# Kernel tuning notes

Measured on AMD Instinct MI355X. Metric: run time of the kernel, lower is better.

Reference implementation:

```python
import jax, jax.numpy as jnp
import numpy as np

LN2 = float(np.log(2.0))

def shifted_softplus(x):
    return jax.nn.softplus(x) - LN2

def setup_inputs() -> dict:
    key = jax.random.key(0)
    ks = jax.random.split(key, 6)
    B, N, K, G, F = 32, 256, 64, 64, 128
    features = jax.random.normal(ks[0], (B, N, F), dtype=jnp.float32)
    rbf_expansion = jax.random.uniform(ks[1], (B, N, K, G), dtype=jnp.float32)
    neighbor_list = jax.random.randint(ks[2], (B, N, K), 0, N).astype(jnp.int64)
    neighbor_mask = jnp.ones((B, N, K), dtype=jnp.float32)
    W1 = jax.random.normal(ks[3], (G, F), dtype=jnp.float32) * (1.0 / np.sqrt(G))
    b1 = jnp.zeros((F,), dtype=jnp.float32)
    W2 = jax.random.normal(ks[4], (F, F), dtype=jnp.float32) * (1.0 / np.sqrt(F))
    b2 = jnp.zeros((F,), dtype=jnp.float32)
    return {"features": features, "rbf_expansion": rbf_expansion,
            "neighbor_list": neighbor_list, "neighbor_mask": neighbor_mask,
            "W1": W1, "b1": b1, "W2": W2, "b2": b2}

def reference(features, rbf_expansion, neighbor_list, neighbor_mask, W1, b1, W2, b2):
    B, N, K = neighbor_list.shape
    F = features.shape[2]
    # filter-generating MLP: linear + shifted softplus, then linear (no activation)
    h = shifted_softplus(jnp.einsum('bnkg,gf->bnkf', rbf_expansion, W1) + b1)
    conv_filter = jnp.einsum('bnkf,fh->bnkh', h, W2) + b2  # [B,N,K,F]
    # gather neighbor features along bead axis
    idx = neighbor_list.reshape(B, N * K)[..., None]  # [B, N*K, 1]
    neighbor_features = jnp.take_along_axis(features, idx, axis=1).reshape(B, N, K, F)
    conv_features = neighbor_features * conv_filter * neighbor_mask[:, :, :, None]
    aggregated_features = jnp.sum(conv_features, axis=2)  # [B, N, F]
    return aggregated_features
```

## Files before the change

### kernel.cpp

```cpp
#include <hip/hip_runtime.h>

#define LN2f 0.69314718055994530942f

typedef short s16x8 __attribute__((ext_vector_type(8)));
typedef float f32x4 __attribute__((ext_vector_type(4)));

constexpr int Bdim = 32, Ndim = 256, Kn = 64, Gdim = 64, Fdim = 128;
constexpr int TPB = 8;
constexpr int LDH = Fdim + 8;

__device__ __forceinline__ short f2bf(float x) {
    unsigned u = __float_as_uint(x);
    u = (u + 0x7FFFu + ((u >> 16) & 1u)) >> 16;
    return (short)u;
}
__device__ __forceinline__ s16x8 cvt8(float4 u, float4 v) {
    s16x8 a;
    a[0]=f2bf(u.x); a[1]=f2bf(u.y); a[2]=f2bf(u.z); a[3]=f2bf(u.w);
    a[4]=f2bf(v.x); a[5]=f2bf(v.y); a[6]=f2bf(v.z); a[7]=f2bf(v.w);
    return a;
}

__global__ __launch_bounds__(256, 2)
void cfconv_kernel(const float* __restrict__ features,
                   const float* __restrict__ rbf,
                   const int*   __restrict__ nbr,
                   const float* __restrict__ mask,
                   const float* __restrict__ W1,
                   const float* __restrict__ b1,
                   const float* __restrict__ W2,
                   const float* __restrict__ b2,
                   float* __restrict__ out)
{
    __shared__ short h_lds[Kn][LDH];
    __shared__ int   nbr_lds[2][Kn];
    __shared__ float mask_lds[2][Kn];

    const int tid  = threadIdx.x;
    const int lane = tid & 63;
    const int w    = tid >> 6;
    const int l16  = lane & 15;
    const int grp  = lane >> 4;

    s16x8 w1f[2][2];
    #pragma unroll
    for (int ks = 0; ks < 2; ++ks)
      #pragma unroll
      for (int nf = 0; nf < 2; ++nf) {
        int g0 = ks*32 + grp*8;
        int f  = w*32 + nf*16 + l16;
        #pragma unroll
        for (int j = 0; j < 8; ++j)
          w1f[ks][nf][j] = f2bf(W1[(g0+j)*Fdim + f]);
      }
    s16x8 w2f[4][2];
    #pragma unroll
    for (int ks = 0; ks < 4; ++ks)
      #pragma unroll
      for (int nf = 0; nf < 2; ++nf) {
        int g0 = ks*32 + grp*8;
        int f  = w*32 + nf*16 + l16;
        #pragma unroll
        for (int j = 0; j < 8; ++j)
          w2f[ks][nf][j] = f2bf(W2[(g0+j)*Fdim + f]);
      }
    float b1v[2], b2v[2];
    #pragma unroll
    for (int nf = 0; nf < 2; ++nf) {
      int f = w*32 + nf*16 + l16;
      b1v[nf] = b1[f];
      b2v[nf] = b2[f];
    }

    const int bn0 = blockIdx.x * TPB;

    float4 st[8][2];
    {
        const float* rb = rbf + (size_t)bn0 * (Kn * Gdim) + l16 * Gdim + grp * 8;
        #pragma unroll
        for (int i = 0; i < 8; ++i) {
            const float* p = rb + (i >> 1) * 16 * Gdim + (i & 1) * 32;
            st[i][0] = *(const float4*)p;
            st[i][1] = *(const float4*)(p + 4);
        }
    }

    for (int t = 0; t < TPB; ++t) {
        const int bn = bn0 + t;
        const int b  = bn >> 8;

        if (tid < Kn) {
            nbr_lds[t & 1][tid]  = nbr[bn*Kn + tid];
            mask_lds[t & 1][tid] = mask[bn*Kn + tid];
        }

        s16x8 af[4][2];
        #pragma unroll
        for (int m = 0; m < 4; ++m) {
            af[m][0] = cvt8(st[m*2][0],   st[m*2][1]);
            af[m][1] = cvt8(st[m*2+1][0], st[m*2+1][1]);
        }
        if (t + 1 < TPB) {
            const float* rbn = rbf + (size_t)(bn + 1) * (Kn * Gdim) + l16 * Gdim + grp * 8;
            #pragma unroll
            for (int i = 0; i < 8; ++i) {
                const float* p = rbn + (i >> 1) * 16 * Gdim + (i & 1) * 32;
                st[i][0] = *(const float4*)p;
                st[i][1] = *(const float4*)(p + 4);
            }
        }

        f32x4 acc[4][2];
        #pragma unroll
        for (int m = 0; m < 4; ++m)
          #pragma unroll
          for (int nf = 0; nf < 2; ++nf)
            acc[m][nf] = (f32x4){0.f, 0.f, 0.f, 0.f};
        #pragma unroll
        for (int m = 0; m < 4; ++m)
          #pragma unroll
          for (int ks = 0; ks < 2; ++ks)
            #pragma unroll
            for (int nf = 0; nf < 2; ++nf)
              acc[m][nf] = __builtin_amdgcn_mfma_f32_16x16x32_bf16(
                               af[m][ks], w1f[ks][nf], acc[m][nf], 0, 0, 0);

        #pragma unroll
        for (int m = 0; m < 4; ++m)
          #pragma unroll
          for (int nf = 0; nf < 2; ++nf)
            #pragma unroll
            for (int r = 0; r < 4; ++r) {
              float x  = acc[m][nf][r] + b1v[nf];
              float sp = fmaxf(x, 0.f) + __logf(1.f + __expf(-fabsf(x))) - LN2f;
              int row = m*16 + grp*4 + r;
              int col = w*32 + nf*16 + l16;
              h_lds[row][col] = f2bf(sp);
            }
        __syncthreads();

        #pragma unroll
        for (int m = 0; m < 4; ++m)
          #pragma unroll
          for (int nf = 0; nf < 2; ++nf)
            acc[m][nf] = (f32x4){0.f, 0.f, 0.f, 0.f};
        #pragma unroll
        for (int m = 0; m < 4; ++m) {
          #pragma unroll
          for (int ks = 0; ks < 4; ++ks) {
            s16x8 a = *(const s16x8*)&h_lds[m*16 + l16][ks*32 + grp*8];
            #pragma unroll
            for (int nf = 0; nf < 2; ++nf)
              acc[m][nf] = __builtin_amdgcn_mfma_f32_16x16x32_bf16(
                               a, w2f[ks][nf], acc[m][nf], 0, 0, 0);
          }
        }
        __syncthreads();

        const float* fb = features + (size_t)b * (Ndim * Fdim);
        float o0 = 0.f, o1 = 0.f;
        #pragma unroll
        for (int m = 0; m < 4; ++m)
          #pragma unroll
          for (int r = 0; r < 4; ++r) {
            int   kn  = m*16 + grp*4 + r;
            int   idx = nbr_lds[t & 1][kn];
            float mk  = mask_lds[t & 1][kn];
            const float* fr = fb + idx * Fdim;
            int f0 = w*32 + l16;
            float flt0 = (acc[m][0][r] + b2v[0]) * mk;
            float flt1 = (acc[m][1][r] + b2v[1]) * mk;
            o0 += fr[f0]      * flt0;
            o1 += fr[f0 + 16] * flt1;
          }
        o0 += __shfl_xor(o0, 16); o0 += __shfl_xor(o0, 32);
        o1 += __shfl_xor(o1, 16); o1 += __shfl_xor(o1, 32);
        float ov = (grp == 0) ? o0 : o1;
        if (grp < 2)
            out[(size_t)bn * Fdim + w*32 + grp*16 + l16] = ov;
    }
}

extern "C" void kernel_launch(void* const* d_in, const int* in_sizes, int n_in,
                              void* d_out, int out_size, void* d_ws, size_t ws_size,
                              hipStream_t stream) {
    const float* features = (const float*)d_in[0];
    const float* rbf      = (const float*)d_in[1];
    const int*   nbr      = (const int*)  d_in[2];
    const float* mask     = (const float*)d_in[3];
    const float* W1       = (const float*)d_in[4];
    const float* b1       = (const float*)d_in[5];
    const float* W2       = (const float*)d_in[6];
    const float* b2       = (const float*)d_in[7];
    float* out = (float*)d_out;

    dim3 grid(Bdim * Ndim / TPB), block(256);
    hipLaunchKernelGGL(cfconv_kernel, grid, block, 0, stream,
                       features, rbf, nbr, mask, W1, b1, W2, b2, out);
}
```

Before: 269.2 us.

## Use packed bf16 convert and overlap neighbor gathers with second GEMM halves

Replaces the software float-to-bf16 rounding with the hardware v_cvt_pk_bf16_f32 instruction, packing two values per conversion. The second GEMM is split into two halves of rows, and the neighbor feature gathers for each half are issued before its MFMAs so global load latency hides behind matrix work. Accumulation uses split partial sums, and the trailing barrier moves to the end of the iteration. This adds register pressure for the prefetched gather values, which could affect occupancy under the launch bound of 2.

```diff
diff --git a/kernel.cpp b/kernel.cpp
--- a/kernel.cpp
+++ b/kernel.cpp
@@ -4,21 +4,21 @@
 
 typedef short s16x8 __attribute__((ext_vector_type(8)));
 typedef float f32x4 __attribute__((ext_vector_type(4)));
+typedef unsigned int u32;
+typedef unsigned int u32x4 __attribute__((ext_vector_type(4)));
 
 constexpr int Bdim = 32, Ndim = 256, Kn = 64, Gdim = 64, Fdim = 128;
 constexpr int TPB = 8;
 constexpr int LDH = Fdim + 8;
 
-__device__ __forceinline__ short f2bf(float x) {
-    unsigned u = __float_as_uint(x);
-    u = (u + 0x7FFFu + ((u >> 16) & 1u)) >> 16;
-    return (short)u;
+__device__ __forceinline__ u32 cvtpk(float lo, float hi) {
+    u32 r;
+    asm("v_cvt_pk_bf16_f32 %0, %1, %2" : "=v"(r) : "v"(lo), "v"(hi));
+    return r;
 }
 __device__ __forceinline__ s16x8 cvt8(float4 u, float4 v) {
-    s16x8 a;
-    a[0]=f2bf(u.x); a[1]=f2bf(u.y); a[2]=f2bf(u.z); a[3]=f2bf(u.w);
-    a[4]=f2bf(v.x); a[5]=f2bf(v.y); a[6]=f2bf(v.z); a[7]=f2bf(v.w);
-    return a;
+    u32x4 q = { cvtpk(u.x, u.y), cvtpk(u.z, u.w), cvtpk(v.x, v.y), cvtpk(v.z, v.w) };
+    return __builtin_bit_cast(s16x8, q);
 }
 
 __global__ __launch_bounds__(256, 2)
@@ -41,6 +41,7 @@
     const int w    = tid >> 6;
     const int l16  = lane & 15;
     const int grp  = lane >> 4;
+    const int f0   = w * 32 + l16;
 
     s16x8 w1f[2][2];
     #pragma unroll
@@ -49,9 +50,11 @@
       for (int nf = 0; nf < 2; ++nf) {
         int g0 = ks*32 + grp*8;
         int f  = w*32 + nf*16 + l16;
-        #pragma unroll
-        for (int j = 0; j < 8; ++j)
-          w1f[ks][nf][j] = f2bf(W1[(g0+j)*Fdim + f]);
+        u32x4 q;
+        #pragma unroll
+        for (int j2 = 0; j2 < 4; ++j2)
+          q[j2] = cvtpk(W1[(g0 + 2*j2)*Fdim + f], W1[(g0 + 2*j2 + 1)*Fdim + f]);
+        w1f[ks][nf] = __builtin_bit_cast(s16x8, q);
       }
     s16x8 w2f[4][2];
     #pragma unroll
@@ -60,9 +63,11 @@
       for (int nf = 0; nf < 2; ++nf) {
         int g0 = ks*32 + grp*8;
         int f  = w*32 + nf*16 + l16;
-        #pragma unroll
-        for (int j = 0; j < 8; ++j)
-          w2f[ks][nf][j] = f2bf(W2[(g0+j)*Fdim + f]);
+        u32x4 q;
+        #pragma unroll
+        for (int j2 = 0; j2 < 4; ++j2)
+          q[j2] = cvtpk(W2[(g0 + 2*j2)*Fdim + f], W2[(g0 + 2*j2 + 1)*Fdim + f]);
+        w2f[ks][nf] = __builtin_bit_cast(s16x8, q);
       }
     float b1v[2], b2v[2];
     #pragma unroll
@@ -88,10 +93,11 @@
     for (int t = 0; t < TPB; ++t) {
         const int bn = bn0 + t;
         const int b  = bn >> 8;
+        const int cb = t & 1;
 
         if (tid < Kn) {
-            nbr_lds[t & 1][tid]  = nbr[bn*Kn + tid];
-            mask_lds[t & 1][tid] = mask[bn*Kn + tid];
+            nbr_lds[cb][tid]  = nbr[bn*Kn + tid];
+            mask_lds[cb][tid] = mask[bn*Kn + tid];
         }
 
         s16x8 af[4][2];
@@ -128,56 +134,94 @@
         #pragma unroll
         for (int m = 0; m < 4; ++m)
           #pragma unroll
-          for (int nf = 0; nf < 2; ++nf)
-            #pragma unroll
-            for (int r = 0; r < 4; ++r) {
-              float x  = acc[m][nf][r] + b1v[nf];
-              float sp = fmaxf(x, 0.f) + __logf(1.f + __expf(-fabsf(x))) - LN2f;
-              int row = m*16 + grp*4 + r;
-              int col = w*32 + nf*16 + l16;
-              h_lds[row][col] = f2bf(sp);
-            }
+          for (int r = 0; r < 4; ++r) {
+            float x0 = acc[m][0][r] + b1v[0];
+            float x1 = acc[m][1][r] + b1v[1];
+            float s0 = fmaxf(x0, 0.f) + __logf(1.f + __expf(-fabsf(x0))) - LN2f;
+            float s1 = fmaxf(x1, 0.f) + __logf(1.f + __expf(-fabsf(x1))) - LN2f;
+            u32 p = cvtpk(s0, s1);
+            int row = m*16 + grp*4 + r;
+            h_lds[row][f0]      = (short)(p & 0xffffu);
+            h_lds[row][f0 + 16] = (short)(p >> 16);
+          }
         __syncthreads();
 
-        #pragma unroll
-        for (int m = 0; m < 4; ++m)
-          #pragma unroll
-          for (int nf = 0; nf < 2; ++nf)
-            acc[m][nf] = (f32x4){0.f, 0.f, 0.f, 0.f};
-        #pragma unroll
-        for (int m = 0; m < 4; ++m) {
+        const float* fb = features + (size_t)b * (Ndim * Fdim);
+
+        float fa0[8], fa1[8];
+        #pragma unroll
+        for (int i = 0; i < 8; ++i) {
+            int kn  = (i >> 2)*16 + grp*4 + (i & 3);
+            const float* fr = fb + (size_t)nbr_lds[cb][kn] * Fdim;
+            fa0[i] = fr[f0];
+            fa1[i] = fr[f0 + 16];
+        }
+
+        f32x4 c2[2][2];
+        #pragma unroll
+        for (int m = 0; m < 2; ++m) {
+          c2[m][0] = (f32x4){0.f,0.f,0.f,0.f};
+          c2[m][1] = (f32x4){0.f,0.f,0.f,0.f};
           #pragma unroll
           for (int ks = 0; ks < 4; ++ks) {
             s16x8 a = *(const s16x8*)&h_lds[m*16 + l16][ks*32 + grp*8];
-            #pragma unroll
-            for (int nf = 0; nf < 2; ++nf)
-              acc[m][nf] = __builtin_amdgcn_mfma_f32_16x16x32_bf16(
-                               a, w2f[ks][nf], acc[m][nf], 0, 0, 0);
+            c2[m][0] = __builtin_amdgcn_mfma_f32_16x16x32_bf16(a, w2f[ks][0], c2[m][0], 0,0,0);
+            c2[m][1] = __builtin_amdgcn_mfma_f32_16x16x32_bf16(a, w2f[ks][1], c2[m][1], 0,0,0);
           }
         }
-        __syncthreads();
-
-        const float* fb = features + (size_t)b * (Ndim * Fdim);
-        float o0 = 0.f, o1 = 0.f;
-        #pragma unroll
-        for (int m = 0; m < 4; ++m)
-          #pragma unroll
-          for (int r = 0; r < 4; ++r) {
-            int   kn  = m*16 + grp*4 + r;
-            int   idx = nbr_lds[t & 1][kn];
-            float mk  = mask_lds[t & 1][kn];
-            const float* fr = fb + idx * Fdim;
-            int f0 = w*32 + l16;
-            float flt0 = (acc[m][0][r] + b2v[0]) * mk;
-            float flt1 = (acc[m][1][r] + b2v[1]) * mk;
-            o0 += fr[f0]      * flt0;
-            o1 += fr[f0 + 16] * flt1;
+
+        float fb0[8], fb1[8];
+        #pragma unroll
+        for (int i = 0; i < 8; ++i) {
+            int kn  = (2 + (i >> 2))*16 + grp*4 + (i & 3);
+            const float* fr = fb + (size_t)nbr_lds[cb][kn] * Fdim;
+            fb0[i] = fr[f0];
+            fb1[i] = fr[f0 + 16];
+        }
+
+        float o0 = 0.f, o1 = 0.f, p0 = 0.f, p1 = 0.f;
+        #pragma unroll
+        for (int i = 0; i < 8; ++i) {
+            int m = i >> 2, r = i & 3;
+            int kn = m*16 + grp*4 + r;
+            float mk = mask_lds[cb][kn];
+            if (i & 1) { p0 += fa0[i] * ((c2[m][0][r] + b2v[0]) * mk);
+                         p1 += fa1[i] * ((c2[m][1][r] + b2v[1]) * mk); }
+            else       { o0 += fa0[i] * ((c2[m][0][r] + b2v[0]) * mk);
+                         o1 += fa1[i] * ((c2[m][1][r] + b2v[1]) * mk); }
+        }
+
+        #pragma unroll
+        for (int m = 0; m < 2; ++m) {
+          c2[m][0] = (f32x4){0.f,0.f,0.f,0.f};
+          c2[m][1] = (f32x4){0.f,0.f,0.f,0.f};
+          #pragma unroll
+          for (int ks = 0; ks < 4; ++ks) {
+            s16x8 a = *(const s16x8*)&h_lds[(m+2)*16 + l16][ks*32 + grp*8];
+            c2[m][0] = __builtin_amdgcn_mfma_f32_16x16x32_bf16(a, w2f[ks][0], c2[m][0], 0,0,0);
+            c2[m][1] = __builtin_amdgcn_mfma_f32_16x16x32_bf16(a, w2f[ks][1], c2[m][1], 0,0,0);
           }
+        }
+
+        #pragma unroll
+        for (int i = 0; i < 8; ++i) {
+            int m = i >> 2, r = i & 3;
+            int kn = (m+2)*16 + grp*4 + r;
+            float mk = mask_lds[cb][kn];
+            if (i & 1) { p0 += fb0[i] * ((c2[m][0][r] + b2v[0]) * mk);
+                         p1 += fb1[i] * ((c2[m][1][r] + b2v[1]) * mk); }
+            else       { o0 += fb0[i] * ((c2[m][0][r] + b2v[0]) * mk);
+                         o1 += fb1[i] * ((c2[m][1][r] + b2v[1]) * mk); }
+        }
+        o0 += p0; o1 += p1;
+
         o0 += __shfl_xor(o0, 16); o0 += __shfl_xor(o0, 32);
         o1 += __shfl_xor(o1, 16); o1 += __shfl_xor(o1, 32);
         float ov = (grp == 0) ? o0 : o1;
         if (grp < 2)
             out[(size_t)bn * Fdim + w*32 + grp*16 + l16] = ov;
+
+        __syncthreads();
     }
 }
 
```

New measurement: 261.5 us. 1.03x faster.
